# Kernel optimization log

Hardware: AMD Instinct MI355X
Metric: run time of the kernel (lower is better)

## Reference

```python
import jax, jax.numpy as jnp
import numpy as np

B, H, E, R, T = 2048, 512, 300, 512, 50


def setup_inputs() -> dict:
    key = jax.random.key(0)
    ks = jax.random.split(key, 12)
    s = 0.02  # xavier-ish scale for params
    return {
        "x": jax.random.normal(ks[0], (B, E), jnp.float32),
        "h_enc": jax.random.normal(ks[1], (B, R), jnp.float32),
        "phi_history": jax.random.normal(ks[2], (T, B, H), jnp.float32),
        "cell_history": jax.random.normal(ks[3], (T, B, H), jnp.float32),
        "h_summ": jax.random.normal(ks[4], (B, H), jnp.float32),
        "c_summ": jax.random.normal(ks[5], (B, H), jnp.float32),
        "W_w": jax.random.normal(ks[6], (4 * H, H + E), jnp.float32) * s,
        "W_b": jnp.zeros((4 * H,), jnp.float32),
        "v_w": jax.random.normal(ks[7], (1, H), jnp.float32) * s,
        "v_b": jnp.zeros((1,), jnp.float32),
        "lq_w": jax.random.normal(ks[8], (H, R), jnp.float32) * s,
        "lq_b": jnp.zeros((H,), jnp.float32),
        "lk_w": jax.random.normal(ks[9], (H, H), jnp.float32) * s,
        "lk_b": jnp.zeros((H,), jnp.float32),
        "ls_w": jax.random.normal(ks[10], (H, H), jnp.float32) * s,
        "ls_b": jnp.zeros((H,), jnp.float32),
    }


def reference(x, h_enc, phi_history, cell_history, h_summ, c_summ,
              W_w, W_b, v_w, v_b, lq_w, lq_b, lk_w, lk_b, ls_w, ls_b):
    Hd = h_summ.shape[-1]
    # [T,B,H] -> [B,T,H] (torch.stack(...).transpose(0,1))
    phi = jnp.transpose(phi_history, (1, 0, 2))
    cell = jnp.transpose(cell_history, (1, 0, 2))
    # additive attention over cached history
    q = h_enc @ lq_w.T + lq_b                       # [B,H]
    k = jnp.einsum('bth,ah->bta', phi, lk_w) + lk_b  # [B,T,H]
    su = h_summ @ ls_w.T + ls_b                     # [B,H]
    e = jnp.tanh(q[:, None, :] + k + su[:, None, :])
    scores = jnp.einsum('bth,oh->bto', e, v_w)[..., 0] + v_b[0]  # [B,T]
    p = jax.nn.softmax(scores, axis=-1)
    h_s = jnp.einsum('bt,bth->bh', p, phi)
    c_s = jnp.einsum('bt,bth->bh', p, cell)
    # fused LSTM gates on [h_summ, x]
    gates = jnp.concatenate([h_s, x], axis=1) @ W_w.T + W_b  # [B,4H]
    f_t = jax.nn.sigmoid(gates[:, :Hd])
    o_t = jax.nn.sigmoid(gates[:, Hd:2 * Hd])
    i_t = jax.nn.sigmoid(gates[:, 2 * Hd:3 * Hd])
    ch_t = jnp.tanh(gates[:, 3 * Hd:])
    c_ctrl = f_t * c_s + i_t * ch_t
    h_ctrl = o_t * jnp.tanh(c_ctrl)
    return h_ctrl
```

## Files before the change

### kernel.cpp

```cpp
#include <hip/hip_runtime.h>
#include <math.h>

#define Bm 2048
#define Hm 512
#define Em 300
#define Tm 50
#define KWm 812
#define KWp 832

typedef unsigned short u16;
typedef unsigned int u32;
typedef __attribute__((ext_vector_type(8))) short short8;
typedef __attribute__((ext_vector_type(8))) u16 ushort8v;
typedef __attribute__((ext_vector_type(4))) float f32x4;

__device__ __forceinline__ float sigmoidf_(float x) { return 1.f / (1.f + __expf(-x)); }
__device__ __forceinline__ float tanhfast(float x) { return 1.f - 2.f / (__expf(2.f * x) + 1.f); }

__device__ __forceinline__ u16 bfr(float x) {
    union { float f; u32 u; } c; c.f = x;
    u32 u = c.u;
    u += 0x7FFFu + ((u >> 16) & 1u);
    return (u16)(u >> 16);
}
__device__ __forceinline__ ushort8v cvt8(const float* __restrict__ p) {
    f32x4 v0 = *(const f32x4*)p;
    f32x4 v1 = *(const f32x4*)(p + 4);
    ushort8v r;
    r[0] = bfr(v0[0]); r[1] = bfr(v0[1]); r[2] = bfr(v0[2]); r[3] = bfr(v0[3]);
    r[4] = bfr(v1[0]); r[5] = bfr(v1[1]); r[6] = bfr(v1[2]); r[7] = bfr(v1[3]);
    return r;
}

__device__ __forceinline__ void gload16(const u16* g, u16* l) {
    __builtin_amdgcn_global_load_lds((const __attribute__((address_space(1))) void*)g,
                                     (__attribute__((address_space(3))) void*)l, 16, 0, 0);
}

__global__ __launch_bounds__(256) void k_pack_phi(
        const float* __restrict__ phi, u16* __restrict__ phib) {
    const size_t nvec = (size_t)Tm * Bm * 512 / 8;
    for (size_t i = (size_t)blockIdx.x * 256 + threadIdx.x; i < nvec;
         i += (size_t)gridDim.x * 256)
        *(ushort8v*)&phib[i * 8] = cvt8(phi + i * 8);
}

__global__ __launch_bounds__(256) void k_pack(
        const float* __restrict__ henc, const float* __restrict__ hsum,
        const float* __restrict__ lq, const float* __restrict__ ls,
        const float* __restrict__ Ww, const float* __restrict__ x,
        const float* __restrict__ lkw,
        u16* __restrict__ Aq, u16* __restrict__ Wq,
        u16* __restrict__ Wg, u16* __restrict__ Xb, u16* __restrict__ lkwb) {
    const int job = blockIdx.y;
    const int r = blockIdx.x;
    const int tid = threadIdx.x;
    if (job == 0) {
        for (int c = tid; c < 1024; c += 256) {
            float v = (c < 512) ? henc[(size_t)r * 512 + c] : hsum[(size_t)r * 512 + (c - 512)];
            Aq[(size_t)r * 1024 + c] = bfr(v);
        }
    } else if (job == 1) {
        if (r < 512)
            for (int c = tid; c < 1024; c += 256) {
                float v = (c < 512) ? lq[(size_t)r * 512 + c] : ls[(size_t)r * 512 + (c - 512)];
                Wq[(size_t)r * 1024 + c] = bfr(v);
            }
    } else if (job == 2) {
        for (int c = tid; c < KWp; c += 256)
            Wg[(size_t)r * KWp + c] = (c < KWm) ? bfr(Ww[(size_t)r * KWm + c]) : (u16)0;
    } else if (job == 3) {
        for (int c = 512 + tid; c < KWp; c += 256)
            Xb[(size_t)r * KWp + c] = (c < KWm) ? bfr(x[(size_t)r * Em + (c - 512)]) : (u16)0;
    } else {
        if (r < 512)
            for (int c = tid; c < 512; c += 256)
                lkwb[(size_t)r * 512 + c] = bfr(lkw[(size_t)r * 512 + c]);
    }
}

__global__ __launch_bounds__(256) void k_qs_mfma(
        const u16* __restrict__ Aq, const u16* __restrict__ Wq,
        const float* __restrict__ lqb, const float* __restrict__ lsb,
        const float* __restrict__ lkb, float* __restrict__ qs) {
    __shared__ u16 Asl[64 * 32];
    __shared__ u16 Bsl[64 * 32];
    const int m0 = blockIdx.x * 64, n0 = blockIdx.y * 64;
    const int tid = threadIdx.x, lane = tid & 63, wid = tid >> 6;
    const int wr = wid >> 1, wc = wid & 1;
    const int l15 = lane & 15, l4 = lane >> 4;
    const int srow = (wid << 4) + (lane >> 2);
    const int gchunk = (lane & 3) ^ ((srow >> 1) & 3);
    f32x4 acc[2][2];
    #pragma unroll
    for (int i = 0; i < 2; ++i)
        #pragma unroll
        for (int j = 0; j < 2; ++j) acc[i][j] = (f32x4){0.f, 0.f, 0.f, 0.f};

    for (int k0 = 0; k0 < 1024; k0 += 32) {
        __syncthreads();
        gload16(Aq + (size_t)(m0 + srow) * 1024 + k0 + gchunk * 8, &Asl[wid * 512]);
        gload16(Wq + (size_t)(n0 + srow) * 1024 + k0 + gchunk * 8, &Bsl[wid * 512]);
        __syncthreads();
        short8 af[2], bf[2];
        #pragma unroll
        for (int mf = 0; mf < 2; ++mf) {
            int r = wr * 32 + mf * 16 + l15;
            af[mf] = *(const short8*)&Asl[r * 32 + (l4 ^ ((r >> 1) & 3)) * 8];
        }
        #pragma unroll
        for (int nf = 0; nf < 2; ++nf) {
            int r = wc * 32 + nf * 16 + l15;
            bf[nf] = *(const short8*)&Bsl[r * 32 + (l4 ^ ((r >> 1) & 3)) * 8];
        }
        #pragma unroll
        for (int mf = 0; mf < 2; ++mf)
            #pragma unroll
            for (int nf = 0; nf < 2; ++nf)
                acc[mf][nf] = __builtin_amdgcn_mfma_f32_16x16x32_bf16(
                                  af[mf], bf[nf], acc[mf][nf], 0, 0, 0);
    }
    #pragma unroll
    for (int mf = 0; mf < 2; ++mf)
        #pragma unroll
        for (int nf = 0; nf < 2; ++nf)
            #pragma unroll
            for (int reg = 0; reg < 4; ++reg) {
                int b = m0 + wr * 32 + mf * 16 + l4 * 4 + reg;
                int h = n0 + wc * 32 + nf * 16 + l15;
                qs[(size_t)b * Hm + h] = acc[mf][nf][reg] + lqb[h] + lsb[h] + lkb[h];
            }
}

__global__ __launch_bounds__(256) void k_scores_mfma(
        const u16* __restrict__ phib, const u16* __restrict__ lkwb,
        const float* __restrict__ qs2, const float* __restrict__ vw,
        float* __restrict__ scores) {
    __shared__ u16 Asl[128 * 64];
    __shared__ u16 Bsl[128 * 64];
    const int d  = blockIdx.x;
    const int wg = (d & 7) * 400 + (d >> 3);
    const int n0 = (wg & 3) << 7;
    const int m0 = (wg >> 2) << 7;
    const int t  = m0 >> 11;
    const int b0 = m0 & (Bm - 1);
    const int tid = threadIdx.x, lane = tid & 63, wid = tid >> 6;
    const int wr = wid >> 1, wc = wid & 1;
    const int l15 = lane & 15, l4 = lane >> 4;
    const int srow_in = lane >> 3;
    const int schunk  = (lane & 7) ^ srow_in;

    f32x4 acc[4][4];
    #pragma unroll
    for (int i = 0; i < 4; ++i)
        #pragma unroll
        for (int j = 0; j < 4; ++j) acc[i][j] = (f32x4){0.f, 0.f, 0.f, 0.f};

    for (int kt = 0; kt < 8; ++kt) {
        const int k0 = kt << 6;
        __syncthreads();
        #pragma unroll
        for (int j = 0; j < 4; ++j) {
            int r = (wid << 5) + (j << 3) + srow_in;
            gload16(phib + (size_t)(m0 + r) * 512 + k0 + schunk * 8,
                    &Asl[((wid << 5) + (j << 3)) * 64]);
            gload16(lkwb + (size_t)(n0 + r) * 512 + k0 + schunk * 8,
                    &Bsl[((wid << 5) + (j << 3)) * 64]);
        }
        __syncthreads();
        short8 af[4][2], bf[4][2];
        #pragma unroll
        for (int mf = 0; mf < 4; ++mf) {
            int r = wr * 64 + mf * 16 + l15;
            #pragma unroll
            for (int ks = 0; ks < 2; ++ks) {
                int c = ks * 4 + l4;
                af[mf][ks] = *(const short8*)&Asl[r * 64 + (c ^ (r & 7)) * 8];
            }
        }
        #pragma unroll
        for (int nf = 0; nf < 4; ++nf) {
            int r = wc * 64 + nf * 16 + l15;
            #pragma unroll
            for (int ks = 0; ks < 2; ++ks) {
                int c = ks * 4 + l4;
                bf[nf][ks] = *(const short8*)&Bsl[r * 64 + (c ^ (r & 7)) * 8];
            }
        }
        __builtin_amdgcn_s_setprio(1);
        #pragma unroll
        for (int ks = 0; ks < 2; ++ks)
            #pragma unroll
            for (int mf = 0; mf < 4; ++mf)
                #pragma unroll
                for (int nf = 0; nf < 4; ++nf)
                    acc[mf][nf] = __builtin_amdgcn_mfma_f32_16x16x32_bf16(
                                      af[mf][ks], bf[nf][ks], acc[mf][nf], 0, 0, 0);
        __builtin_amdgcn_s_setprio(0);
    }

    float vws[4];
    int av[4];
    #pragma unroll
    for (int nf = 0; nf < 4; ++nf) {
        av[nf] = n0 + wc * 64 + nf * 16 + l15;
        vws[nf] = vw[av[nf]];
    }
    #pragma unroll
    for (int mf = 0; mf < 4; ++mf) {
        #pragma unroll
        for (int reg = 0; reg < 4; ++reg) {
            int b = b0 + wr * 64 + mf * 16 + l4 * 4 + reg;
            const float* q = qs2 + (size_t)b * Hm;
            float s = 0.f;
            #pragma unroll
            for (int nf = 0; nf < 4; ++nf)
                s = fmaf(tanhfast(acc[mf][nf][reg] + q[av[nf]]), vws[nf], s);
            #pragma unroll
            for (int o = 1; o < 16; o <<= 1) s += __shfl_xor(s, o);
            if (l15 == 0) atomicAdd(&scores[(size_t)b * Tm + t], s);
        }
    }
}

__global__ __launch_bounds__(256) void k_attn(
        const u16* __restrict__ phib, const float* __restrict__ cell,
        const float* __restrict__ scores,
        u16* __restrict__ Xb, float* __restrict__ cs) {
    __shared__ float p[Tm];
    const int b = blockIdx.x;
    const int tid = threadIdx.x;
    if (tid < 64) {
        float s = (tid < Tm) ? scores[(size_t)b * Tm + tid] : -INFINITY;
        float m = s;
        #pragma unroll
        for (int o = 32; o; o >>= 1) m = fmaxf(m, __shfl_xor(m, o));
        float ex = (tid < Tm) ? __expf(s - m) : 0.f;
        float sum = ex;
        #pragma unroll
        for (int o = 32; o; o >>= 1) sum += __shfl_xor(sum, o);
        if (tid < Tm) p[tid] = ex / sum;
    }
    __syncthreads();
    const int c0 = tid * 2;
    float ah0 = 0.f, ah1 = 0.f, ac0 = 0.f, ac1 = 0.f;
    for (int t = 0; t < Tm; ++t) {
        float w = p[t];
        const size_t rb = ((size_t)t * Bm + b) * 512 + c0;
        u32 ph2 = *(const u32*)&phib[rb];
        float2 ce2 = *(const float2*)&cell[rb];
        float p0 = __uint_as_float(ph2 << 16);
        float p1 = __uint_as_float(ph2 & 0xFFFF0000u);
        ah0 = fmaf(w, p0, ah0);
        ah1 = fmaf(w, p1, ah1);
        ac0 = fmaf(w, ce2.x, ac0);
        ac1 = fmaf(w, ce2.y, ac1);
    }
    *(u32*)&Xb[(size_t)b * KWp + c0] = (u32)bfr(ah0) | ((u32)bfr(ah1) << 16);
    *(float2*)&cs[(size_t)b * Hm + c0] = make_float2(ac0, ac1);
}

__global__ __launch_bounds__(256) void k_gates_mfma(
        const u16* __restrict__ Xb, const u16* __restrict__ Wg,
        float* __restrict__ gates) {
    __shared__ u16 Asl[64 * 32];
    __shared__ u16 Bsl[128 * 32];
    const int m0 = blockIdx.x * 64, n0 = blockIdx.y * 128;
    const int tid = threadIdx.x, lane = tid & 63, wid = tid >> 6;
    const int wr = wid >> 1, wc = wid & 1;
    const int l15 = lane & 15, l4 = lane >> 4;
    const int srow = (wid << 4) + (lane >> 2);
    const int gchunkA = (lane & 3) ^ ((srow >> 1) & 3);
    f32x4 acc[2][4];
    #pragma unroll
    for (int i = 0; i < 2; ++i)
        #pragma unroll
        for (int j = 0; j < 4; ++j) acc[i][j] = (f32x4){0.f, 0.f, 0.f, 0.f};

    for (int k0 = 0; k0 < KWp; k0 += 32) {
        __syncthreads();
        gload16(Xb + (size_t)(m0 + srow) * KWp + k0 + gchunkA * 8, &Asl[wid * 512]);
        #pragma unroll
        for (int j = 0; j < 2; ++j) {
            int brow = (wid << 5) + (j << 4) + (lane >> 2);
            int gchunkB = (lane & 3) ^ ((brow >> 1) & 3);
            gload16(Wg + (size_t)(n0 + brow) * KWp + k0 + gchunkB * 8,
                    &Bsl[wid * 1024 + j * 512]);
        }
        __syncthreads();
        short8 af[2], bf[4];
        #pragma unroll
        for (int mf = 0; mf < 2; ++mf) {
            int r = wr * 32 + mf * 16 + l15;
            af[mf] = *(const short8*)&Asl[r * 32 + (l4 ^ ((r >> 1) & 3)) * 8];
        }
        #pragma unroll
        for (int nf = 0; nf < 4; ++nf) {
            int r = wc * 64 + nf * 16 + l15;
            bf[nf] = *(const short8*)&Bsl[r * 32 + (l4 ^ ((r >> 1) & 3)) * 8];
        }
        #pragma unroll
        for (int mf = 0; mf < 2; ++mf)
            #pragma unroll
            for (int nf = 0; nf < 4; ++nf)
                acc[mf][nf] = __builtin_amdgcn_mfma_f32_16x16x32_bf16(
                                  af[mf], bf[nf], acc[mf][nf], 0, 0, 0);
    }
    #pragma unroll
    for (int mf = 0; mf < 2; ++mf)
        #pragma unroll
        for (int nf = 0; nf < 4; ++nf)
            #pragma unroll
            for (int reg = 0; reg < 4; ++reg) {
                int b = m0 + wr * 32 + mf * 16 + l4 * 4 + reg;
                int n = n0 + wc * 64 + nf * 16 + l15;
                gates[(size_t)b * 2048 + n] = acc[mf][nf][reg];
            }
}

__global__ __launch_bounds__(256) void k_lstm(
        const float* __restrict__ gates, const float* __restrict__ Wb,
        const float* __restrict__ cs, float* __restrict__ out) {
    const int idx = blockIdx.x * 256 + threadIdx.x;
    const int b = idx >> 9, h = idx & 511;
    const float* g = gates + (size_t)b * 2048;
    float f  = sigmoidf_(g[h]        + Wb[h]);
    float o  = sigmoidf_(g[512 + h]  + Wb[512 + h]);
    float ii = sigmoidf_(g[1024 + h] + Wb[1024 + h]);
    float ch = tanhfast( g[1536 + h] + Wb[1536 + h]);
    float c  = f * cs[idx] + ii * ch;
    out[idx] = o * tanhfast(c);
}

extern "C" void kernel_launch(void* const* d_in, const int* in_sizes, int n_in,
                              void* d_out, int out_size, void* d_ws, size_t ws_size,
                              hipStream_t stream) {
    const float* x      = (const float*)d_in[0];
    const float* h_enc  = (const float*)d_in[1];
    const float* phi    = (const float*)d_in[2];
    const float* cell   = (const float*)d_in[3];
    const float* h_summ = (const float*)d_in[4];
    const float* W_w    = (const float*)d_in[6];
    const float* W_b    = (const float*)d_in[7];
    const float* v_w    = (const float*)d_in[8];
    const float* lq_w   = (const float*)d_in[10];
    const float* lq_b   = (const float*)d_in[11];
    const float* lk_w   = (const float*)d_in[12];
    const float* lk_b   = (const float*)d_in[13];
    const float* ls_w   = (const float*)d_in[14];
    const float* ls_b   = (const float*)d_in[15];
    float* out = (float*)d_out;

    char* w = (char*)d_ws;
    u16*   phib   = (u16*)  (w);
    float* gates  = (float*)(w);
    float* qs     = (float*)(w + 104857600);
    float* scores = (float*)(w + 109051904);
    float* cs     = (float*)(w + 109461504);
    u16*   Aq     = (u16*)  (w + 113655808);
    u16*   Wq     = (u16*)  (w + 117850112);
    u16*   Wg     = (u16*)  (w + 118898688);
    u16*   Xb     = (u16*)  (w + 122306560);
    u16*   lkwb   = (u16*)  (w + 125714432);

    hipMemsetAsync(scores, 0, (size_t)Bm * Tm * sizeof(float), stream);
    k_pack<<<dim3(2048, 5), 256, 0, stream>>>(h_enc, h_summ, lq_w, ls_w, W_w, x, lk_w,
                                              Aq, Wq, Wg, Xb, lkwb);
    k_pack_phi<<<dim3(2048), 256, 0, stream>>>(phi, phib);
    k_qs_mfma<<<dim3(Bm / 64, Hm / 64), 256, 0, stream>>>(Aq, Wq, lq_b, ls_b, lk_b, qs);
    k_scores_mfma<<<dim3(3200), 256, 0, stream>>>(phib, lkwb, qs, v_w, scores);
    k_attn<<<dim3(Bm), 256, 0, stream>>>(phib, cell, scores, Xb, cs);
    k_gates_mfma<<<dim3(Bm / 64, 2048 / 128), 256, 0, stream>>>(Xb, Wg, gates);
    k_lstm<<<dim3((Bm * Hm) / 256), 256, 0, stream>>>(gates, W_b, cs, out);
}
```

Baseline: 310.5 us.

## Fuse phi bf16 conversion into scores GEMM A-tile loads

```diff
diff --git a/kernel.cpp b/kernel.cpp
--- a/kernel.cpp
+++ b/kernel.cpp
@@ -23,9 +23,7 @@
     u += 0x7FFFu + ((u >> 16) & 1u);
     return (u16)(u >> 16);
 }
-__device__ __forceinline__ ushort8v cvt8(const float* __restrict__ p) {
-    f32x4 v0 = *(const f32x4*)p;
-    f32x4 v1 = *(const f32x4*)(p + 4);
+__device__ __forceinline__ ushort8v pk8(f32x4 v0, f32x4 v1) {
     ushort8v r;
     r[0] = bfr(v0[0]); r[1] = bfr(v0[1]); r[2] = bfr(v0[2]); r[3] = bfr(v0[3]);
     r[4] = bfr(v1[0]); r[5] = bfr(v1[1]); r[6] = bfr(v1[2]); r[7] = bfr(v1[3]);
@@ -35,14 +33,6 @@
 __device__ __forceinline__ void gload16(const u16* g, u16* l) {
     __builtin_amdgcn_global_load_lds((const __attribute__((address_space(1))) void*)g,
                                      (__attribute__((address_space(3))) void*)l, 16, 0, 0);
-}
-
-__global__ __launch_bounds__(256) void k_pack_phi(
-        const float* __restrict__ phi, u16* __restrict__ phib) {
-    const size_t nvec = (size_t)Tm * Bm * 512 / 8;
-    for (size_t i = (size_t)blockIdx.x * 256 + threadIdx.x; i < nvec;
-         i += (size_t)gridDim.x * 256)
-        *(ushort8v*)&phib[i * 8] = cvt8(phi + i * 8);
 }
 
 __global__ __launch_bounds__(256) void k_pack(
@@ -133,9 +123,9 @@
 }
 
 __global__ __launch_bounds__(256) void k_scores_mfma(
-        const u16* __restrict__ phib, const u16* __restrict__ lkwb,
+        const float* __restrict__ phi, const u16* __restrict__ lkwb,
         const float* __restrict__ qs2, const float* __restrict__ vw,
-        float* __restrict__ scores) {
+        float* __restrict__ scores, u16* __restrict__ phib) {
     __shared__ u16 Asl[128 * 64];
     __shared__ u16 Bsl[128 * 64];
     const int d  = blockIdx.x;
@@ -147,8 +137,10 @@
     const int tid = threadIdx.x, lane = tid & 63, wid = tid >> 6;
     const int wr = wid >> 1, wc = wid & 1;
     const int l15 = lane & 15, l4 = lane >> 4;
-    const int srow_in = lane >> 3;
-    const int schunk  = (lane & 7) ^ srow_in;
+    const int rin = lane >> 3;
+    const int ca  = lane & 7;
+    const int schunkB = ca ^ rin;
+    const bool wb = (n0 == 0);
 
     f32x4 acc[4][4];
     #pragma unroll
@@ -161,11 +153,19 @@
         __syncthreads();
         #pragma unroll
         for (int j = 0; j < 4; ++j) {
-            int r = (wid << 5) + (j << 3) + srow_in;
-            gload16(phib + (size_t)(m0 + r) * 512 + k0 + schunk * 8,
-                    &Asl[((wid << 5) + (j << 3)) * 64]);
-            gload16(lkwb + (size_t)(n0 + r) * 512 + k0 + schunk * 8,
+            int r = (wid << 5) + (j << 3) + rin;
+            gload16(lkwb + (size_t)(n0 + r) * 512 + k0 + schunkB * 8,
                     &Bsl[((wid << 5) + (j << 3)) * 64]);
+        }
+        #pragma unroll
+        for (int u = 0; u < 4; ++u) {
+            int ra = (wid << 5) + (u << 3) + rin;
+            const float* src = phi + (size_t)(m0 + ra) * 512 + k0 + ca * 8;
+            f32x4 a0 = *(const f32x4*)src;
+            f32x4 a1 = *(const f32x4*)(src + 4);
+            ushort8v c8 = pk8(a0, a1);
+            if (wb) *(ushort8v*)(phib + (size_t)(m0 + ra) * 512 + k0 + ca * 8) = c8;
+            *(ushort8v*)&Asl[ra * 64 + ((ca ^ rin) << 3)] = c8;
         }
         __syncthreads();
         short8 af[4][2], bf[4][2];
@@ -366,9 +366,8 @@
     hipMemsetAsync(scores, 0, (size_t)Bm * Tm * sizeof(float), stream);
     k_pack<<<dim3(2048, 5), 256, 0, stream>>>(h_enc, h_summ, lq_w, ls_w, W_w, x, lk_w,
                                               Aq, Wq, Wg, Xb, lkwb);
-    k_pack_phi<<<dim3(2048), 256, 0, stream>>>(phi, phib);
     k_qs_mfma<<<dim3(Bm / 64, Hm / 64), 256, 0, stream>>>(Aq, Wq, lq_b, ls_b, lk_b, qs);
-    k_scores_mfma<<<dim3(3200), 256, 0, stream>>>(phib, lkwb, qs, v_w, scores);
+    k_scores_mfma<<<dim3(3200), 256, 0, stream>>>(phi, lkwb, qs, v_w, scores, phib);
     k_attn<<<dim3(Bm), 256, 0, stream>>>(phib, cell, scores, Xb, cs);
     k_gates_mfma<<<dim3(Bm / 64, 2048 / 128), 256, 0, stream>>>(Xb, Wg, gates);
     k_lstm<<<dim3((Bm * Hm) / 256), 256, 0, stream>>>(gates, W_b, cs, out);
```

After: 375.0 us. +20.7%, slower.
